# Performance work log

Hardware: AMD Instinct MI355X
Metric: run time of the kernel (lower is better)

## Reference

```python
import jax, jax.numpy as jnp
import numpy as np

N = 10000   # nodes
E = 320000  # edges
D = 256     # in_dim == hidden_dim
H = 4       # heads
DK = 64     # head dim
BN_EPS = 1e-5


def _relu6(x):
    return jnp.clip(x, 0.0, 6.0)


def setup_inputs() -> dict:
    key = jax.random.key(0)
    ks = jax.random.split(key, 16)
    rn = lambda k, shape, s=0.05: jax.random.normal(k, shape, dtype=jnp.float32) * s
    return {
        "v": jax.random.normal(ks[0], (N, D), dtype=jnp.float32),
        "WQ": rn(ks[1], (D, D)), "bQ": jnp.zeros((D,), jnp.float32),
        "WK": rn(ks[2], (D, D)), "bK": jnp.zeros((D,), jnp.float32),
        "WV": rn(ks[3], (D, D)), "bV": jnp.zeros((D,), jnp.float32),
        "Wo": rn(ks[4], (D, D)), "bo": jnp.zeros((D,), jnp.float32),
        "W1": rn(ks[5], (D, 64)), "b1": jnp.zeros((64,), jnp.float32),
        "W2": rn(ks[6], (64, D)), "b2": jnp.zeros((D,), jnp.float32),
        "gamma": jnp.ones((D,), jnp.float32),
        "beta": jnp.zeros((D,), jnp.float32),
        "src": jax.random.randint(ks[7], (E,), 0, N),
        "dst": jax.random.randint(ks[8], (E,), 0, N),
    }


def reference(v, WQ, bQ, WK, bK, WV, bV, Wo, bo, W1, b1, W2, b2, gamma, beta, src, dst):
    ones_e = jnp.ones((E,), jnp.float32)
    # center weighting: softmax over (in_degree + out_degree)
    deg = (jax.ops.segment_sum(ones_e, src, num_segments=N)
           + jax.ops.segment_sum(ones_e, dst, num_segments=N))
    center = jax.nn.softmax(deg)                      # [N]
    mV = v * center[:, None]                          # [N, D]

    q = (mV @ WQ + bQ).reshape(N, H, DK)
    k = (mV @ WK + bK).reshape(N, H, DK)
    vv = (mV @ WV + bV).reshape(N, H, DK)

    # edge score: dot(k[src], q[dst]) per head, clamped scaled exp
    score = jnp.einsum('ehd,ehd->eh', k[src], q[dst])  # [E, H]
    s = jnp.exp(jnp.clip(score / np.sqrt(DK), -5.0, 5.0))

    wv = jax.ops.segment_sum(vv[src] * s[:, :, None], dst, num_segments=N)  # [N,H,DK]
    z = jax.ops.segment_sum(s, dst, num_segments=N)                         # [N,H]

    o = (wv / z[:, :, None]).reshape(N, D) @ Wo + bo   # output projection

    # BatchNorm1d (training-mode batch stats, biased var) + ReLU6
    mean = jnp.mean(o, axis=0)
    var = jnp.mean((o - mean) ** 2, axis=0)
    x = _relu6(gamma * (o - mean) / jnp.sqrt(var + BN_EPS) + beta)

    # SE block: Linear -> ReLU6 -> Linear -> HardSwish
    se = _relu6(x @ W1 + b1) @ W2 + b2
    se = se * _relu6(se + 3.0) / 6.0

    return se * x + v
```

## Files before the change

kernel.cpp:

```cpp
#include <hip/hip_runtime.h>
#include <math.h>

#define N_NODES 10000
#define N_EDGES 320000
#define DIM 256
#define ND ((size_t)N_NODES * DIM)

typedef float f32x4 __attribute__((ext_vector_type(4)));
typedef short s16x8 __attribute__((ext_vector_type(8)));

__device__ __forceinline__ float relu6f(float x) { return fminf(fmaxf(x, 0.f), 6.f); }

__device__ __forceinline__ short f2bf(float x) {
  unsigned u = __builtin_bit_cast(unsigned, x);
  unsigned r = (u + 0x7fffu + ((u >> 16) & 1u)) >> 16;
  return (short)r;
}
__device__ __forceinline__ float bf2f(short b) {
  unsigned u = ((unsigned)(unsigned short)b) << 16;
  return __builtin_bit_cast(float, u);
}
__device__ __forceinline__ float bflo(unsigned u) {
  return __builtin_bit_cast(float, u << 16);
}
__device__ __forceinline__ float bfhi(unsigned u) {
  return __builtin_bit_cast(float, u & 0xffff0000u);
}

__global__ void k_deg(const int* __restrict__ src, const int* __restrict__ dst,
                      int* __restrict__ outc, int* __restrict__ inc) {
  int e = blockIdx.x * 256 + threadIdx.x;
  if (e < N_EDGES) {
    atomicAdd(&outc[src[e]], 1);
    atomicAdd(&inc[dst[e]], 1);
  }
}

__global__ void k_expsum(const int* __restrict__ inc, const int* __restrict__ outc,
                         double* __restrict__ Zd) {
  int i = blockIdx.x * 256 + threadIdx.x;
  int lane = threadIdx.x & 63;
  double e = 0.0;
  if (i < N_NODES) e = exp((double)(inc[i] + outc[i]));
#pragma unroll
  for (int off = 1; off < 64; off <<= 1) e += __shfl_xor(e, off);
  if (lane == 0) atomicAdd(Zd, e);
}

__global__ __launch_bounds__(256) void k_wsplit(
    const float* __restrict__ Wa, const float* __restrict__ Wb,
    const float* __restrict__ Wc, const float* __restrict__ Wd,
    short* __restrict__ Whi, short* __restrict__ Wlo) {
  const float* W = (blockIdx.y == 0) ? Wa : (blockIdx.y == 1) ? Wb
                   : (blockIdx.y == 2) ? Wc : Wd;
  short* hi = Whi + (size_t)blockIdx.y * 65536;
  short* lo = Wlo + (size_t)blockIdx.y * 65536;
  __shared__ float tile[64][65];
  int t = threadIdx.x;
  int tk = (blockIdx.x >> 2) * 64, tn = (blockIdx.x & 3) * 64;
  int r = t >> 4, c4 = (t & 15) * 4;
#pragma unroll
  for (int p = 0; p < 4; p++) {
    float4 v4 = *(const float4*)(W + (size_t)(tk + p * 16 + r) * 256 + tn + c4);
    tile[p * 16 + r][c4 + 0] = v4.x;
    tile[p * 16 + r][c4 + 1] = v4.y;
    tile[p * 16 + r][c4 + 2] = v4.z;
    tile[p * 16 + r][c4 + 3] = v4.w;
  }
  __syncthreads();
  int nl = t >> 2, q = t & 3;
  s16x8 h0, h1, l0, l1;
#pragma unroll
  for (int j = 0; j < 8; j++) {
    float x = tile[q * 16 + j][nl];
    short hb = f2bf(x);
    h0[j] = hb; l0[j] = f2bf(x - bf2f(hb));
  }
#pragma unroll
  for (int j = 0; j < 8; j++) {
    float x = tile[q * 16 + 8 + j][nl];
    short hb = f2bf(x);
    h1[j] = hb; l1[j] = f2bf(x - bf2f(hb));
  }
  size_t base = (size_t)(tn + nl) * 256 + tk + q * 16;
  *(s16x8*)(hi + base) = h0;
  *(s16x8*)(hi + base + 8) = h1;
  *(s16x8*)(lo + base) = l0;
  *(s16x8*)(lo + base + 8) = l1;
}

__global__ __launch_bounds__(256) void k_wsplit_t(
    const float* __restrict__ W, short* __restrict__ hi, short* __restrict__ lo,
    int K, int N) {
  __shared__ float tile[64][65];
  int t = threadIdx.x;
  int tk = blockIdx.x * 64, tn = blockIdx.y * 64;
  int r = t >> 4, c4 = (t & 15) * 4;
#pragma unroll
  for (int p = 0; p < 4; p++) {
    float4 v4 = *(const float4*)(W + (size_t)(tk + p * 16 + r) * N + tn + c4);
    tile[p * 16 + r][c4 + 0] = v4.x;
    tile[p * 16 + r][c4 + 1] = v4.y;
    tile[p * 16 + r][c4 + 2] = v4.z;
    tile[p * 16 + r][c4 + 3] = v4.w;
  }
  __syncthreads();
  int nl = t >> 2, q = t & 3;
  s16x8 h0, h1, l0, l1;
#pragma unroll
  for (int j = 0; j < 8; j++) {
    float x = tile[q * 16 + j][nl];
    short hb = f2bf(x);
    h0[j] = hb; l0[j] = f2bf(x - bf2f(hb));
  }
#pragma unroll
  for (int j = 0; j < 8; j++) {
    float x = tile[q * 16 + 8 + j][nl];
    short hb = f2bf(x);
    h1[j] = hb; l1[j] = f2bf(x - bf2f(hb));
  }
  size_t base = (size_t)(tn + nl) * K + tk + q * 16;
  *(s16x8*)(hi + base) = h0;
  *(s16x8*)(hi + base + 8) = h1;
  *(s16x8*)(lo + base) = l0;
  *(s16x8*)(lo + base + 8) = l1;
}

template <int MULC, int KVMODE>
__global__ __launch_bounds__(256) void k_gemm_mfma(
    const float* __restrict__ A, const short* __restrict__ Whi,
    const short* __restrict__ Wlo, const float* __restrict__ b0,
    const float* __restrict__ b1, const float* __restrict__ b2,
    const int* __restrict__ inc, const int* __restrict__ outc,
    const float* __restrict__ logzf, float* __restrict__ Qout,
    unsigned short* __restrict__ KVout, float* __restrict__ Cbase, int M) {
  const float* bias = (blockIdx.z == 0) ? b0 : (blockIdx.z == 1) ? b1 : b2;
  const short* whi = Whi + (size_t)blockIdx.z * 65536;
  const short* wlo = Wlo + (size_t)blockIdx.z * 65536;

  __shared__ __align__(16) short Ah[64][40];
  __shared__ __align__(16) short Al[64][40];
  __shared__ __align__(16) short Bh[128][40];
  __shared__ __align__(16) short Bl[128][40];

  int tid = threadIdx.x;
  int lane = tid & 63, wid = tid >> 6;
  int wm = wid >> 1, wn = wid & 1;
  int m0 = blockIdx.x * 64;
  int n0g = blockIdx.y * 128;

  f32x4 acc[2][4];
#pragma unroll
  for (int i = 0; i < 2; i++)
#pragma unroll
    for (int j = 0; j < 4; j++) acc[i][j] = (f32x4){0.f, 0.f, 0.f, 0.f};

  int sa_row = tid >> 2, sa_seg = tid & 3;
  int sb_row = tid >> 1, sb_seg = tid & 1;
  float cmul = 1.f;
  if (MULC) {
    int m = m0 + sa_row;
    cmul = (m < M) ? __expf((float)(inc[m] + outc[m]) - logzf[0]) : 0.f;
  }

  for (int k0 = 0; k0 < 256; k0 += 32) {
    __syncthreads();
    {
      int m = m0 + sa_row;
      float4 x0 = make_float4(0.f, 0.f, 0.f, 0.f), x1 = x0;
      if (m < M) {
        const float* ap = A + (size_t)m * 256 + k0 + sa_seg * 8;
        x0 = *(const float4*)ap;
        x1 = *(const float4*)(ap + 4);
        if (MULC) {
          x0.x *= cmul; x0.y *= cmul; x0.z *= cmul; x0.w *= cmul;
          x1.x *= cmul; x1.y *= cmul; x1.z *= cmul; x1.w *= cmul;
        }
      }
      s16x8 h, l;
      float xs[8] = {x0.x, x0.y, x0.z, x0.w, x1.x, x1.y, x1.z, x1.w};
#pragma unroll
      for (int j = 0; j < 8; j++) {
        short hb = f2bf(xs[j]);
        h[j] = hb; l[j] = f2bf(xs[j] - bf2f(hb));
      }
      *(s16x8*)&Ah[sa_row][sa_seg * 8] = h;
      *(s16x8*)&Al[sa_row][sa_seg * 8] = l;
    }
    {
      size_t gb = (size_t)(n0g + sb_row) * 256 + k0 + sb_seg * 16;
      *(s16x8*)&Bh[sb_row][sb_seg * 16] = *(const s16x8*)(whi + gb);
      *(s16x8*)&Bh[sb_row][sb_seg * 16 + 8] = *(const s16x8*)(whi + gb + 8);
      *(s16x8*)&Bl[sb_row][sb_seg * 16] = *(const s16x8*)(wlo + gb);
      *(s16x8*)&Bl[sb_row][sb_seg * 16 + 8] = *(const s16x8*)(wlo + gb + 8);
    }
    __syncthreads();
    int arow0 = wm * 32 + (lane & 15);
    int kc = (lane >> 4) * 8;
    s16x8 ah[2], al[2], bh[4], bl[4];
#pragma unroll
    for (int mf = 0; mf < 2; mf++) {
      ah[mf] = *(const s16x8*)&Ah[arow0 + mf * 16][kc];
      al[mf] = *(const s16x8*)&Al[arow0 + mf * 16][kc];
    }
    int brow0 = wn * 64 + (lane & 15);
#pragma unroll
    for (int nf = 0; nf < 4; nf++) {
      bh[nf] = *(const s16x8*)&Bh[brow0 + nf * 16][kc];
      bl[nf] = *(const s16x8*)&Bl[brow0 + nf * 16][kc];
    }
#pragma unroll
    for (int mf = 0; mf < 2; mf++)
#pragma unroll
      for (int nf = 0; nf < 4; nf++) {
        acc[mf][nf] = __builtin_amdgcn_mfma_f32_16x16x32_bf16(ah[mf], bh[nf], acc[mf][nf], 0, 0, 0);
        acc[mf][nf] = __builtin_amdgcn_mfma_f32_16x16x32_bf16(al[mf], bh[nf], acc[mf][nf], 0, 0, 0);
        acc[mf][nf] = __builtin_amdgcn_mfma_f32_16x16x32_bf16(ah[mf], bl[nf], acc[mf][nf], 0, 0, 0);
      }
  }

  int colq = lane & 15, rowq = (lane >> 4) * 4;
  bool isq = (KVMODE == 0) || (blockIdx.z == 0);
  int kvoff = (blockIdx.z == 1) ? 0 : 256;
#pragma unroll
  for (int mf = 0; mf < 2; mf++) {
#pragma unroll
    for (int nf = 0; nf < 4; nf++) {
      int n = wn * 64 + nf * 16 + colq;
      float bv = bias[n0g + n];
#pragma unroll
      for (int j = 0; j < 4; j++) {
        int m = m0 + wm * 32 + mf * 16 + rowq + j;
        if (m >= M) continue;
        float val = acc[mf][nf][j] + bv;
        if (isq) {
          float* C = (KVMODE == 1) ? Qout : Cbase;
          C[(size_t)m * 256 + n0g + n] = val;
        } else {
          KVout[(size_t)m * 512 + kvoff + n0g + n] = (unsigned short)f2bf(val);
        }
      }
    }
  }
}

__global__ void k_scan(const int* __restrict__ cnt, int* __restrict__ rowptr,
                       int* __restrict__ nextp, const double* __restrict__ Zd,
                       float* __restrict__ logzf) {
  __shared__ int wsum[16];
  __shared__ int carry_s;
  int tid = threadIdx.x, lane = tid & 63, wid = tid >> 6;
  if (tid == 0) {
    carry_s = 0;
    logzf[0] = (float)log(Zd[0]);
  }
  __syncthreads();
  for (int base = 0; base < N_NODES; base += 1024) {
    int i = base + tid;
    int v = (i < N_NODES) ? cnt[i] : 0;
    int x = v;
#pragma unroll
    for (int off = 1; off < 64; off <<= 1) {
      int t = __shfl_up(x, off);
      if (lane >= off) x += t;
    }
    if (lane == 63) wsum[wid] = x;
    __syncthreads();
    if (wid == 0 && lane < 16) {
      int wv = wsum[lane];
#pragma unroll
      for (int off = 1; off < 16; off <<= 1) {
        int t = __shfl_up(wv, off);
        if (lane >= off) wv += t;
      }
      wsum[lane] = wv;
    }
    __syncthreads();
    int carry = carry_s;
    int wadd = (wid > 0) ? wsum[wid - 1] : 0;
    int excl = carry + wadd + x - v;
    if (i < N_NODES) {
      rowptr[i] = excl;
      nextp[i] = excl;
    }
    __syncthreads();
    if (tid == 1023) carry_s = excl + v;
    __syncthreads();
  }
  if (tid == 0) rowptr[N_NODES] = carry_s;
}

__global__ void k_fill(const int* __restrict__ src, const int* __restrict__ dst,
                       int* __restrict__ nextp, int* __restrict__ csr_src) {
  int e = blockIdx.x * 256 + threadIdx.x;
  if (e < N_EDGES) {
    int pos = atomicAdd(&nextp[dst[e]], 1);
    csr_src[pos] = src[e];
  }
}

__global__ __launch_bounds__(256) void k_edgeagg(
    const int* __restrict__ rowptr, const int* __restrict__ csr_src,
    const float* __restrict__ q, const unsigned short* __restrict__ kv,
    float* __restrict__ att) {
  int lane = threadIdx.x & 63, wid = threadIdx.x >> 6;
  int n = blockIdx.x * 4 + wid;
  int beg = rowptr[n], end = rowptr[n + 1];
  float4 qv = *(const float4*)(q + (size_t)n * 256 + lane * 4);
  const unsigned short* kvl = kv + lane * 4;
  float a0 = 0.f, a1 = 0.f, a2 = 0.f, a3 = 0.f, z = 0.f;

#define EDGE_BODY(SRC)                                                        \
  {                                                                           \
    const unsigned short* rp = kvl + (size_t)(SRC) * 512;                     \
    uint2 ku = *(const uint2*)rp;                                             \
    uint2 vu = *(const uint2*)(rp + 256);                                     \
    float p = bflo(ku.x) * qv.x + bfhi(ku.x) * qv.y +                         \
              bflo(ku.y) * qv.z + bfhi(ku.y) * qv.w;                          \
    p += __shfl_xor(p, 1);                                                    \
    p += __shfl_xor(p, 2);                                                    \
    p += __shfl_xor(p, 4);                                                    \
    p += __shfl_xor(p, 8);                                                    \
    float e0 = __expf(fminf(fmaxf(p * 0.125f, -5.f), 5.f));                   \
    a0 = fmaf(e0, bflo(vu.x), a0);                                            \
    a1 = fmaf(e0, bfhi(vu.x), a1);                                            \
    a2 = fmaf(e0, bflo(vu.y), a2);                                            \
    a3 = fmaf(e0, bfhi(vu.y), a3);                                            \
    z += e0;                                                                  \
  }

  for (int base = beg; base < end; base += 64) {
    int idx = base + lane;
    int eid = (idx < end) ? csr_src[idx] : 0;
    int bs = min(64, end - base);
    int j = 0;
    for (; j + 4 <= bs; j += 4) {
      int s0 = __builtin_amdgcn_readlane(eid, j);
      int s1 = __builtin_amdgcn_readlane(eid, j + 1);
      int s2 = __builtin_amdgcn_readlane(eid, j + 2);
      int s3 = __builtin_amdgcn_readlane(eid, j + 3);
      EDGE_BODY(s0); EDGE_BODY(s1); EDGE_BODY(s2); EDGE_BODY(s3);
    }
    for (; j < bs; j++) {
      int s0 = __builtin_amdgcn_readlane(eid, j);
      EDGE_BODY(s0);
    }
  }
#undef EDGE_BODY

  float invz = 1.f / z;
  float4 r;
  r.x = a0 * invz; r.y = a1 * invz; r.z = a2 * invz; r.w = a3 * invz;
  *(float4*)(att + (size_t)n * 256 + lane * 4) = r;
}

__global__ void k_bnstats(const float* __restrict__ o, float* __restrict__ bnsum,
                          float* __restrict__ bnsq) {
  int d = threadIdx.x;
  float s = 0.f, sq = 0.f;
  for (int r = blockIdx.x; r < N_NODES; r += gridDim.x) {
    float val = o[(size_t)r * 256 + d];
    s += val;
    sq = fmaf(val, val, sq);
  }
  atomicAdd(&bnsum[d], s);
  atomicAdd(&bnsq[d], sq);
}

__global__ void k_bnfinal(const float* __restrict__ bnsum, const float* __restrict__ bnsq,
                          const float* __restrict__ gamma, const float* __restrict__ beta,
                          float* __restrict__ scale, float* __restrict__ shift) {
  int d = threadIdx.x;
  float mean = bnsum[d] * (1.f / N_NODES);
  float var = bnsq[d] * (1.f / N_NODES) - mean * mean;
  float istd = rsqrtf(var + 1e-5f);
  float sc = gamma[d] * istd;
  scale[d] = sc;
  shift[d] = beta[d] - mean * sc;
}

__global__ __launch_bounds__(256) void k_se2(
    const float* __restrict__ o, const float* __restrict__ scale,
    const float* __restrict__ shift,
    const short* __restrict__ W1h, const short* __restrict__ W1l,
    const float* __restrict__ b1,
    const short* __restrict__ W2h, const short* __restrict__ W2l,
    const float* __restrict__ b2,
    const float* __restrict__ vin, float* __restrict__ out) {
  __shared__ __align__(16) short xh[64][264];
  __shared__ __align__(16) short xl[64][264];
  __shared__ __align__(16) short hh[64][72];
  __shared__ __align__(16) short hl[64][72];
  __shared__ float vt[64][256];

  int t = threadIdx.x;
  int lane = t & 63, w = t >> 6;
  int m0 = blockIdx.x * 64;

  {
    int r = t >> 2;
    int cb = (t & 3) * 4;
    int gr = m0 + r;
    bool rok = gr < N_NODES;
#pragma unroll
    for (int p = 0; p < 16; p++) {
      int c = cb + p * 16;
      float4 ov = make_float4(0.f, 0.f, 0.f, 0.f), vv = ov;
      if (rok) {
        ov = *(const float4*)(o + (size_t)gr * 256 + c);
        vv = *(const float4*)(vin + (size_t)gr * 256 + c);
      }
      float xs[4];
      xs[0] = relu6f(fmaf(ov.x, scale[c + 0], shift[c + 0]));
      xs[1] = relu6f(fmaf(ov.y, scale[c + 1], shift[c + 1]));
      xs[2] = relu6f(fmaf(ov.z, scale[c + 2], shift[c + 2]));
      xs[3] = relu6f(fmaf(ov.w, scale[c + 3], shift[c + 3]));
#pragma unroll
      for (int j = 0; j < 4; j++) {
        short hb = f2bf(xs[j]);
        xh[r][c + j] = hb;
        xl[r][c + j] = f2bf(xs[j] - bf2f(hb));
      }
      *(float4*)&vt[r][c] = vv;
    }
  }
  __syncthreads();

  int fr = lane & 15, fq = lane >> 4;
  int kc = fq * 8;
  int arow = w * 16 + fr;

  f32x4 acc1[4];
#pragma unroll
  for (int nf = 0; nf < 4; nf++) acc1[nf] = (f32x4){0.f, 0.f, 0.f, 0.f};
#pragma unroll
  for (int ks = 0; ks < 8; ks++) {
    s16x8 ah = *(const s16x8*)&xh[arow][ks * 32 + kc];
    s16x8 al = *(const s16x8*)&xl[arow][ks * 32 + kc];
#pragma unroll
    for (int nf = 0; nf < 4; nf++) {
      size_t bo_ = (size_t)(nf * 16 + fr) * 256 + ks * 32 + kc;
      s16x8 bh = *(const s16x8*)(W1h + bo_);
      s16x8 bl = *(const s16x8*)(W1l + bo_);
      acc1[nf] = __builtin_amdgcn_mfma_f32_16x16x32_bf16(ah, bh, acc1[nf], 0, 0, 0);
      acc1[nf] = __builtin_amdgcn_mfma_f32_16x16x32_bf16(al, bh, acc1[nf], 0, 0, 0);
      acc1[nf] = __builtin_amdgcn_mfma_f32_16x16x32_bf16(ah, bl, acc1[nf], 0, 0, 0);
    }
  }
#pragma unroll
  for (int nf = 0; nf < 4; nf++) {
    int n = nf * 16 + fr;
    float bv = b1[n];
#pragma unroll
    for (int j = 0; j < 4; j++) {
      int row = w * 16 + fq * 4 + j;
      float hv = relu6f(acc1[nf][j] + bv);
      short hb = f2bf(hv);
      hh[row][n] = hb;
      hl[row][n] = f2bf(hv - bf2f(hb));
    }
  }
  __syncthreads();

  f32x4 acc2[16];
#pragma unroll
  for (int nf = 0; nf < 16; nf++) acc2[nf] = (f32x4){0.f, 0.f, 0.f, 0.f};
#pragma unroll
  for (int ks = 0; ks < 2; ks++) {
    s16x8 ah = *(const s16x8*)&hh[arow][ks * 32 + kc];
    s16x8 al = *(const s16x8*)&hl[arow][ks * 32 + kc];
#pragma unroll
    for (int nf = 0; nf < 16; nf++) {
      size_t bo_ = (size_t)(nf * 16 + fr) * 64 + ks * 32 + kc;
      s16x8 bh = *(const s16x8*)(W2h + bo_);
      s16x8 bl = *(const s16x8*)(W2l + bo_);
      acc2[nf] = __builtin_amdgcn_mfma_f32_16x16x32_bf16(ah, bh, acc2[nf], 0, 0, 0);
      acc2[nf] = __builtin_amdgcn_mfma_f32_16x16x32_bf16(al, bh, acc2[nf], 0, 0, 0);
      acc2[nf] = __builtin_amdgcn_mfma_f32_16x16x32_bf16(ah, bl, acc2[nf], 0, 0, 0);
    }
  }
#pragma unroll
  for (int nf = 0; nf < 16; nf++) {
    int col = nf * 16 + fr;
    float bv = b2[col];
#pragma unroll
    for (int j = 0; j < 4; j++) {
      int row = w * 16 + fq * 4 + j;
      int grow = m0 + row;
      if (grow < N_NODES) {
        float se = acc2[nf][j] + bv;
        float hs = se * relu6f(se + 3.f) * (1.f / 6.f);
        float xr = bf2f(xh[row][col]) + bf2f(xl[row][col]);
        out[(size_t)grow * 256 + col] = fmaf(hs, xr, vt[row][col]);
      }
    }
  }
}

extern "C" void kernel_launch(void* const* d_in, const int* in_sizes, int n_in,
                              void* d_out, int out_size, void* d_ws, size_t ws_size,
                              hipStream_t stream) {
  const float* v     = (const float*)d_in[0];
  const float* WQ    = (const float*)d_in[1];
  const float* bQ    = (const float*)d_in[2];
  const float* WK    = (const float*)d_in[3];
  const float* bK    = (const float*)d_in[4];
  const float* WV    = (const float*)d_in[5];
  const float* bV    = (const float*)d_in[6];
  const float* Wo    = (const float*)d_in[7];
  const float* bo    = (const float*)d_in[8];
  const float* W1    = (const float*)d_in[9];
  const float* b1    = (const float*)d_in[10];
  const float* W2    = (const float*)d_in[11];
  const float* b2    = (const float*)d_in[12];
  const float* gamma = (const float*)d_in[13];
  const float* beta  = (const float*)d_in[14];
  const int* srcI    = (const int*)d_in[15];
  const int* dstI    = (const int*)d_in[16];
  float* out = (float*)d_out;

  char* w = (char*)d_ws;
  size_t off = 0;
  auto take = [&](size_t bytes) {
    size_t o = off;
    off += (bytes + 255) & ~(size_t)255;
    return o;
  };
  int* inc      = (int*)(w + take(N_NODES * 4));
  int* outc     = (int*)(w + take(N_NODES * 4));
  float* bnsum  = (float*)(w + take(256 * 4));
  float* bnsq   = (float*)(w + take(256 * 4));
  double* Zd    = (double*)(w + take(8));
  size_t zero_span = off;
  float* logzf  = (float*)(w + take(4));
  float* q      = (float*)(w + take(ND * 4));
  unsigned short* kvb = (unsigned short*)(w + take((size_t)N_NODES * 512 * 2));
  float* scale  = (float*)(w + take(256 * 4));
  float* shift  = (float*)(w + take(256 * 4));
  int* rowptr   = (int*)(w + take((N_NODES + 1) * 4));
  int* nextp    = (int*)(w + take(N_NODES * 4));
  int* csr_src  = (int*)(w + take((size_t)N_EDGES * 4));
  short* Wt_hi  = (short*)(w + take((size_t)4 * 65536 * 2));
  short* Wt_lo  = (short*)(w + take((size_t)4 * 65536 * 2));
  short* W1h    = (short*)(w + take((size_t)16384 * 2));
  short* W1l    = (short*)(w + take((size_t)16384 * 2));
  short* W2h    = (short*)(w + take((size_t)16384 * 2));
  short* W2l    = (short*)(w + take((size_t)16384 * 2));

  float* att = q;
  float* o   = (float*)kvb;

  hipMemsetAsync(w, 0, zero_span, stream);

  k_wsplit<<<dim3(16, 4), dim3(256), 0, stream>>>(WQ, WK, WV, Wo, Wt_hi, Wt_lo);
  k_wsplit_t<<<dim3(4, 1), dim3(256), 0, stream>>>(W1, W1h, W1l, 256, 64);
  k_wsplit_t<<<dim3(1, 4), dim3(256), 0, stream>>>(W2, W2h, W2l, 64, 256);
  k_deg<<<dim3((N_EDGES + 255) / 256), dim3(256), 0, stream>>>(srcI, dstI, outc, inc);
  k_expsum<<<dim3((N_NODES + 255) / 256), dim3(256), 0, stream>>>(inc, outc, Zd);
  k_scan<<<dim3(1), dim3(1024), 0, stream>>>(inc, rowptr, nextp, Zd, logzf);
  k_fill<<<dim3((N_EDGES + 255) / 256), dim3(256), 0, stream>>>(srcI, dstI, nextp, csr_src);

  k_gemm_mfma<1, 1><<<dim3(157, 2, 3), dim3(256), 0, stream>>>(
      v, Wt_hi, Wt_lo, bQ, bK, bV, inc, outc, logzf, q, kvb, nullptr, N_NODES);

  k_edgeagg<<<dim3(N_NODES / 4), dim3(256), 0, stream>>>(rowptr, csr_src, q, kvb, att);

  k_gemm_mfma<0, 0><<<dim3(157, 2, 1), dim3(256), 0, stream>>>(
      att, Wt_hi + (size_t)3 * 65536, Wt_lo + (size_t)3 * 65536,
      bo, bo, bo, nullptr, nullptr, nullptr, nullptr, nullptr, o, N_NODES);

  k_bnstats<<<dim3(240), dim3(256), 0, stream>>>(o, bnsum, bnsq);
  k_bnfinal<<<dim3(1), dim3(256), 0, stream>>>(bnsum, bnsq, gamma, beta, scale, shift);

  k_se2<<<dim3((N_NODES + 63) / 64), dim3(256), 0, stream>>>(
      o, scale, shift, W1h, W1l, b1, W2h, W2l, b2, v, out);
}
```

Measured before the change: 298.9 us.

## Pre-split GEMM inputs to bf16 hi/lo and fuse BN stats into GEMM epilogue

Adds a separate kernel that scales v by the degree-softmax and splits it into bf16 hi/lo once, so the QKV GEMM (three z-slices, two n-blocks) no longer repeats the conversion per block. The edge aggregation now writes its output directly as bf16 hi/lo. The output-projection GEMM accumulates BatchNorm sum and sum-of-squares in its epilogue with shuffles and atomics, and the SE kernel computes scale and shift itself, which removes the separate bnstats and bnfinal kernels. This costs an extra pass over v and extra workspace buffers, and adds atomic contention on the BN accumulators.

```diff
diff --git a/kernel.cpp b/kernel.cpp
--- a/kernel.cpp
+++ b/kernel.cpp
@@ -8,6 +8,7 @@
 
 typedef float f32x4 __attribute__((ext_vector_type(4)));
 typedef short s16x8 __attribute__((ext_vector_type(8)));
+typedef short s16x4 __attribute__((ext_vector_type(4)));
 
 __device__ __forceinline__ float relu6f(float x) { return fminf(fmaxf(x, 0.f), 6.f); }
 
@@ -126,14 +127,35 @@
   *(s16x8*)(lo + base + 8) = l1;
 }
 
-template <int MULC, int KVMODE>
+__global__ __launch_bounds__(256) void k_asplit(
+    const float* __restrict__ v, const int* __restrict__ inc,
+    const int* __restrict__ outc, const float* __restrict__ logzf,
+    short* __restrict__ Ahg, short* __restrict__ Alg) {
+  size_t idx = ((size_t)blockIdx.x * 256 + threadIdx.x) * 4;
+  if (idx >= ND) return;
+  int row = (int)(idx >> 8);
+  float c = __expf((float)(inc[row] + outc[row]) - logzf[0]);
+  float4 x = *(const float4*)(v + idx);
+  float xs[4] = {x.x * c, x.y * c, x.z * c, x.w * c};
+  s16x4 h, l;
+#pragma unroll
+  for (int j = 0; j < 4; j++) {
+    short hb = f2bf(xs[j]);
+    h[j] = hb;
+    l[j] = f2bf(xs[j] - bf2f(hb));
+  }
+  *(s16x4*)(Ahg + idx) = h;
+  *(s16x4*)(Alg + idx) = l;
+}
+
+template <int KVMODE>
 __global__ __launch_bounds__(256) void k_gemm_mfma(
-    const float* __restrict__ A, const short* __restrict__ Whi,
-    const short* __restrict__ Wlo, const float* __restrict__ b0,
-    const float* __restrict__ b1, const float* __restrict__ b2,
-    const int* __restrict__ inc, const int* __restrict__ outc,
-    const float* __restrict__ logzf, float* __restrict__ Qout,
-    unsigned short* __restrict__ KVout, float* __restrict__ Cbase, int M) {
+    const short* __restrict__ Ahg, const short* __restrict__ Alg,
+    const short* __restrict__ Whi, const short* __restrict__ Wlo,
+    const float* __restrict__ b0, const float* __restrict__ b1,
+    const float* __restrict__ b2, float* __restrict__ Qout,
+    unsigned short* __restrict__ KVout, float* __restrict__ Cbase,
+    float* __restrict__ bnsum, float* __restrict__ bnsq, int M) {
   const float* bias = (blockIdx.z == 0) ? b0 : (blockIdx.z == 1) ? b1 : b2;
   const short* whi = Whi + (size_t)blockIdx.z * 65536;
   const short* wlo = Wlo + (size_t)blockIdx.z * 65536;
@@ -157,32 +179,17 @@
 
   int sa_row = tid >> 2, sa_seg = tid & 3;
   int sb_row = tid >> 1, sb_seg = tid & 1;
-  float cmul = 1.f;
-  if (MULC) {
-    int m = m0 + sa_row;
-    cmul = (m < M) ? __expf((float)(inc[m] + outc[m]) - logzf[0]) : 0.f;
-  }
+  const s16x8 zero8 = {0, 0, 0, 0, 0, 0, 0, 0};
 
   for (int k0 = 0; k0 < 256; k0 += 32) {
     __syncthreads();
     {
       int m = m0 + sa_row;
-      float4 x0 = make_float4(0.f, 0.f, 0.f, 0.f), x1 = x0;
+      s16x8 h = zero8, l = zero8;
       if (m < M) {
-        const float* ap = A + (size_t)m * 256 + k0 + sa_seg * 8;
-        x0 = *(const float4*)ap;
-        x1 = *(const float4*)(ap + 4);
-        if (MULC) {
-          x0.x *= cmul; x0.y *= cmul; x0.z *= cmul; x0.w *= cmul;
-          x1.x *= cmul; x1.y *= cmul; x1.z *= cmul; x1.w *= cmul;
-        }
-      }
-      s16x8 h, l;
-      float xs[8] = {x0.x, x0.y, x0.z, x0.w, x1.x, x1.y, x1.z, x1.w};
-#pragma unroll
-      for (int j = 0; j < 8; j++) {
-        short hb = f2bf(xs[j]);
-        h[j] = hb; l[j] = f2bf(xs[j] - bf2f(hb));
+        size_t ga = (size_t)m * 256 + k0 + sa_seg * 8;
+        h = *(const s16x8*)(Ahg + ga);
+        l = *(const s16x8*)(Alg + ga);
       }
       *(s16x8*)&Ah[sa_row][sa_seg * 8] = h;
       *(s16x8*)&Al[sa_row][sa_seg * 8] = l;
@@ -220,25 +227,55 @@
   }
 
   int colq = lane & 15, rowq = (lane >> 4) * 4;
-  bool isq = (KVMODE == 0) || (blockIdx.z == 0);
-  int kvoff = (blockIdx.z == 1) ? 0 : 256;
-#pragma unroll
-  for (int mf = 0; mf < 2; mf++) {
+  if (KVMODE == 1) {
+    bool isq = (blockIdx.z == 0);
+    int kvoff = (blockIdx.z == 1) ? 0 : 256;
+#pragma unroll
+    for (int mf = 0; mf < 2; mf++) {
+#pragma unroll
+      for (int nf = 0; nf < 4; nf++) {
+        int n = wn * 64 + nf * 16 + colq;
+        float bv = bias[n0g + n];
+#pragma unroll
+        for (int j = 0; j < 4; j++) {
+          int m = m0 + wm * 32 + mf * 16 + rowq + j;
+          if (m >= M) continue;
+          float val = acc[mf][nf][j] + bv;
+          if (isq) Qout[(size_t)m * 256 + n0g + n] = val;
+          else KVout[(size_t)m * 512 + kvoff + n0g + n] = (unsigned short)f2bf(val);
+        }
+      }
+    }
+  } else {
+    float cs[4], cq[4];
+#pragma unroll
+    for (int nf = 0; nf < 4; nf++) { cs[nf] = 0.f; cq[nf] = 0.f; }
 #pragma unroll
     for (int nf = 0; nf < 4; nf++) {
       int n = wn * 64 + nf * 16 + colq;
       float bv = bias[n0g + n];
 #pragma unroll
-      for (int j = 0; j < 4; j++) {
-        int m = m0 + wm * 32 + mf * 16 + rowq + j;
-        if (m >= M) continue;
-        float val = acc[mf][nf][j] + bv;
-        if (isq) {
-          float* C = (KVMODE == 1) ? Qout : Cbase;
-          C[(size_t)m * 256 + n0g + n] = val;
-        } else {
-          KVout[(size_t)m * 512 + kvoff + n0g + n] = (unsigned short)f2bf(val);
+      for (int mf = 0; mf < 2; mf++) {
+#pragma unroll
+        for (int j = 0; j < 4; j++) {
+          int m = m0 + wm * 32 + mf * 16 + rowq + j;
+          if (m >= M) continue;
+          float val = acc[mf][nf][j] + bv;
+          Cbase[(size_t)m * 256 + n0g + n] = val;
+          cs[nf] += val;
+          cq[nf] = fmaf(val, val, cq[nf]);
         }
+      }
+    }
+#pragma unroll
+    for (int nf = 0; nf < 4; nf++) {
+      float s = cs[nf], qq = cq[nf];
+      s += __shfl_xor(s, 16); s += __shfl_xor(s, 32);
+      qq += __shfl_xor(qq, 16); qq += __shfl_xor(qq, 32);
+      if (lane < 16) {
+        int n = n0g + wn * 64 + nf * 16 + lane;
+        atomicAdd(&bnsum[n], s);
+        atomicAdd(&bnsq[n], qq);
       }
     }
   }
@@ -302,7 +339,7 @@
 __global__ __launch_bounds__(256) void k_edgeagg(
     const int* __restrict__ rowptr, const int* __restrict__ csr_src,
     const float* __restrict__ q, const unsigned short* __restrict__ kv,
-    float* __restrict__ att) {
+    short* __restrict__ att_h, short* __restrict__ att_l) {
   int lane = threadIdx.x & 63, wid = threadIdx.x >> 6;
   int n = blockIdx.x * 4 + wid;
   int beg = rowptr[n], end = rowptr[n + 1];
@@ -349,39 +386,23 @@
 #undef EDGE_BODY
 
   float invz = 1.f / z;
-  float4 r;
-  r.x = a0 * invz; r.y = a1 * invz; r.z = a2 * invz; r.w = a3 * invz;
-  *(float4*)(att + (size_t)n * 256 + lane * 4) = r;
-}
-
-__global__ void k_bnstats(const float* __restrict__ o, float* __restrict__ bnsum,
-                          float* __restrict__ bnsq) {
-  int d = threadIdx.x;
-  float s = 0.f, sq = 0.f;
-  for (int r = blockIdx.x; r < N_NODES; r += gridDim.x) {
-    float val = o[(size_t)r * 256 + d];
-    s += val;
-    sq = fmaf(val, val, sq);
-  }
-  atomicAdd(&bnsum[d], s);
-  atomicAdd(&bnsq[d], sq);
-}
-
-__global__ void k_bnfinal(const float* __restrict__ bnsum, const float* __restrict__ bnsq,
-                          const float* __restrict__ gamma, const float* __restrict__ beta,
-                          float* __restrict__ scale, float* __restrict__ shift) {
-  int d = threadIdx.x;
-  float mean = bnsum[d] * (1.f / N_NODES);
-  float var = bnsq[d] * (1.f / N_NODES) - mean * mean;
-  float istd = rsqrtf(var + 1e-5f);
-  float sc = gamma[d] * istd;
-  scale[d] = sc;
-  shift[d] = beta[d] - mean * sc;
+  float rs[4] = {a0 * invz, a1 * invz, a2 * invz, a3 * invz};
+  s16x4 h, l;
+#pragma unroll
+  for (int j = 0; j < 4; j++) {
+    short hb = f2bf(rs[j]);
+    h[j] = hb;
+    l[j] = f2bf(rs[j] - bf2f(hb));
+  }
+  size_t base_o = (size_t)n * 256 + lane * 4;
+  *(s16x4*)(att_h + base_o) = h;
+  *(s16x4*)(att_l + base_o) = l;
 }
 
 __global__ __launch_bounds__(256) void k_se2(
-    const float* __restrict__ o, const float* __restrict__ scale,
-    const float* __restrict__ shift,
+    const float* __restrict__ o,
+    const float* __restrict__ bnsum, const float* __restrict__ bnsq,
+    const float* __restrict__ gamma, const float* __restrict__ beta,
     const short* __restrict__ W1h, const short* __restrict__ W1l,
     const float* __restrict__ b1,
     const short* __restrict__ W2h, const short* __restrict__ W2l,
@@ -392,10 +413,21 @@
   __shared__ __align__(16) short hh[64][72];
   __shared__ __align__(16) short hl[64][72];
   __shared__ float vt[64][256];
+  __shared__ float scale_s[256], shift_s[256];
 
   int t = threadIdx.x;
   int lane = t & 63, w = t >> 6;
   int m0 = blockIdx.x * 64;
+
+  {
+    float mean = bnsum[t] * (1.f / N_NODES);
+    float var = bnsq[t] * (1.f / N_NODES) - mean * mean;
+    float istd = rsqrtf(var + 1e-5f);
+    float sc = gamma[t] * istd;
+    scale_s[t] = sc;
+    shift_s[t] = beta[t] - mean * sc;
+  }
+  __syncthreads();
 
   {
     int r = t >> 2;
@@ -411,10 +443,10 @@
         vv = *(const float4*)(vin + (size_t)gr * 256 + c);
       }
       float xs[4];
-      xs[0] = relu6f(fmaf(ov.x, scale[c + 0], shift[c + 0]));
-      xs[1] = relu6f(fmaf(ov.y, scale[c + 1], shift[c + 1]));
-      xs[2] = relu6f(fmaf(ov.z, scale[c + 2], shift[c + 2]));
-      xs[3] = relu6f(fmaf(ov.w, scale[c + 3], shift[c + 3]));
+      xs[0] = relu6f(fmaf(ov.x, scale_s[c + 0], shift_s[c + 0]));
+      xs[1] = relu6f(fmaf(ov.y, scale_s[c + 1], shift_s[c + 1]));
+      xs[2] = relu6f(fmaf(ov.z, scale_s[c + 2], shift_s[c + 2]));
+      xs[3] = relu6f(fmaf(ov.w, scale_s[c + 3], shift_s[c + 3]));
 #pragma unroll
       for (int j = 0; j < 4; j++) {
         short hb = f2bf(xs[j]);
@@ -535,8 +567,10 @@
   float* logzf  = (float*)(w + take(4));
   float* q      = (float*)(w + take(ND * 4));
   unsigned short* kvb = (unsigned short*)(w + take((size_t)N_NODES * 512 * 2));
-  float* scale  = (float*)(w + take(256 * 4));
-  float* shift  = (float*)(w + take(256 * 4));
+  short* Ahg    = (short*)(w + take(ND * 2));
+  short* Alg    = (short*)(w + take(ND * 2));
+  short* att_h  = (short*)(w + take(ND * 2));
+  short* att_l  = (short*)(w + take(ND * 2));
   int* rowptr   = (int*)(w + take((N_NODES + 1) * 4));
   int* nextp    = (int*)(w + take(N_NODES * 4));
   int* csr_src  = (int*)(w + take((size_t)N_EDGES * 4));
@@ -547,8 +581,7 @@
   short* W2h    = (short*)(w + take((size_t)16384 * 2));
   short* W2l    = (short*)(w + take((size_t)16384 * 2));
 
-  float* att = q;
-  float* o   = (float*)kvb;
+  float* o = (float*)kvb;
 
   hipMemsetAsync(w, 0, zero_span, stream);
 
@@ -559,19 +592,17 @@
   k_expsum<<<dim3((N_NODES + 255) / 256), dim3(256), 0, stream>>>(inc, outc, Zd);
   k_scan<<<dim3(1), dim3(1024), 0, stream>>>(inc, rowptr, nextp, Zd, logzf);
   k_fill<<<dim3((N_EDGES + 255) / 256), dim3(256), 0, stream>>>(srcI, dstI, nextp, csr_src);
-
-  k_gemm_mfma<1, 1><<<dim3(157, 2, 3), dim3(256), 0, stream>>>(
-      v, Wt_hi, Wt_lo, bQ, bK, bV, inc, outc, logzf, q, kvb, nullptr, N_NODES);
-
-  k_edgeagg<<<dim3(N_NODES / 4), dim3(256), 0, stream>>>(rowptr, csr_src, q, kvb, att);
-
-  k_gemm_mfma<0, 0><<<dim3(157, 2, 1), dim3(256), 0, stream>>>(
-      att, Wt_hi + (size_t)3 * 65536, Wt_lo + (size_t)3 * 65536,
-      bo, bo, bo, nullptr, nullptr, nullptr, nullptr, nullptr, o, N_NODES);
-
-  k_bnstats<<<dim3(240), dim3(256), 0, stream>>>(o, bnsum, bnsq);
-  k_bnfinal<<<dim3(1), dim3(256), 0, stream>>>(bnsum, bnsq, gamma, beta, scale, shift);
+  k_asplit<<<dim3((int)(ND / 4 / 256)), dim3(256), 0, stream>>>(v, inc, outc, logzf, Ahg, Alg);
+
+  k_gemm_mfma<1><<<dim3(157, 2, 3), dim3(256), 0, stream>>>(
+      Ahg, Alg, Wt_hi, Wt_lo, bQ, bK, bV, q, kvb, nullptr, nullptr, nullptr, N_NODES);
+
+  k_edgeagg<<<dim3(N_NODES / 4), dim3(256), 0, stream>>>(rowptr, csr_src, q, kvb, att_h, att_l);
+
+  k_gemm_mfma<0><<<dim3(157, 2, 1), dim3(256), 0, stream>>>(
+      att_h, att_l, Wt_hi + (size_t)3 * 65536, Wt_lo + (size_t)3 * 65536,
+      bo, bo, bo, nullptr, nullptr, o, bnsum, bnsq, N_NODES);
 
   k_se2<<<dim3((N_NODES + 63) / 64), dim3(256), 0, stream>>>(
-      o, scale, shift, W1h, W1l, b1, W2h, W2l, b2, v, out);
-}
+      o, bnsum, bnsq, gamma, beta, W1h, W1l, b1, W2h, W2l, b2, v, out);
+}
```

Measured after the change: 293.4 us. No clear change (-1.9%).
